# Kernel tuning notes

Measured on AMD Instinct MI355X. Metric: run time of the kernel, lower is better.

## Reference

```python
import jax, jax.numpy as jnp
import numpy as np

B, S, D, H = 4, 2048, 1024, 16
HS = D // H          # head size 64
DF = 4 * D           # ffn hidden 4096
EPS = 1e-5


def _layer_norm(x, g, b):
    mu = jnp.mean(x, axis=-1, keepdims=True)
    var = jnp.var(x, axis=-1, keepdims=True)
    return (x - mu) * jax.lax.rsqrt(var + EPS) * g + b


def setup_inputs() -> dict:
    key = jax.random.key(0)
    ks = jax.random.split(key, 12)
    s_d = 1.0 / np.sqrt(D)
    s_f = 1.0 / np.sqrt(DF)
    return {
        "x": jax.random.normal(ks[0], (B, S, D), jnp.float32),
        # per-head q/k/v projections, batched over heads: [H, D, HS]
        "wq": jax.random.uniform(ks[1], (H, D, HS), jnp.float32, -s_d, s_d),
        "wk": jax.random.uniform(ks[2], (H, D, HS), jnp.float32, -s_d, s_d),
        "wv": jax.random.uniform(ks[3], (H, D, HS), jnp.float32, -s_d, s_d),
        "proj_w": jax.random.uniform(ks[4], (D, D), jnp.float32, -s_d, s_d),
        "proj_b": jax.random.uniform(ks[5], (D,), jnp.float32, -s_d, s_d),
        "ff1_w": jax.random.uniform(ks[6], (D, DF), jnp.float32, -s_d, s_d),
        "ff1_b": jax.random.uniform(ks[7], (DF,), jnp.float32, -s_d, s_d),
        "ff2_w": jax.random.uniform(ks[8], (DF, D), jnp.float32, -s_f, s_f),
        "ff2_b": jax.random.uniform(ks[9], (D,), jnp.float32, -s_f, s_f),
        "ln1_g": jnp.ones((D,), jnp.float32),
        "ln1_b": jnp.zeros((D,), jnp.float32),
        "ln2_g": jnp.ones((D,), jnp.float32),
        "ln2_b": jnp.zeros((D,), jnp.float32),
    }


def reference(x, wq, wk, wv, proj_w, proj_b, ff1_w, ff1_b, ff2_w, ff2_b,
              ln1_g, ln1_b, ln2_g, ln2_b):
    # --- multi-head causal self-attention on ln1(x), all heads batched ---
    h = _layer_norm(x, ln1_g, ln1_b)                      # [B,S,D]
    q = jnp.einsum("bsd,hde->bhse", h, wq)                # [B,H,S,HS]
    k = jnp.einsum("bsd,hde->bhse", h, wk)
    v = jnp.einsum("bsd,hde->bhse", h, wv)
    scale = HS ** -0.5
    scores = jnp.einsum("bhse,bhte->bhst", q, k) * scale  # [B,H,S,S]
    causal = jnp.tril(jnp.ones((S, S), bool))
    scores = jnp.where(causal, scores, jnp.finfo(scores.dtype).min)
    att = jax.nn.softmax(scores, axis=-1)
    o = jnp.einsum("bhst,bhte->bhse", att, v)             # [B,H,S,HS]
    o = o.transpose(0, 2, 1, 3).reshape(B, S, D)          # concat heads
    sa = o @ proj_w + proj_b
    x = x + sa
    # --- FFN on ln2(x) ---
    h2 = _layer_norm(x, ln2_g, ln2_b)
    ff = jax.nn.relu(h2 @ ff1_w + ff1_b) @ ff2_w + ff2_b
    return x + ff
```

## Files before the change

kernel.cpp:

```cpp
#include <hip/hip_runtime.h>
#include <hip/hip_bf16.h>

#define BB 4
#define SS 2048
#define DD 1024
#define HH 16
#define HSZ 64
#define DFF 4096

typedef short short8 __attribute__((ext_vector_type(8)));
typedef float f32x4 __attribute__((ext_vector_type(4)));
typedef unsigned short us4 __attribute__((ext_vector_type(4)));

#define AS1 __attribute__((address_space(1)))
#define AS3 __attribute__((address_space(3)))

__device__ __forceinline__ unsigned short f2bf(float f) {
    return __bfloat16_as_ushort(__float2bfloat16(f));
}
__device__ __forceinline__ float bf2f(unsigned short u) {
    return __uint_as_float(((unsigned int)u) << 16);
}

__global__ __launch_bounds__(256) void pack_all_kernel(
    const float* __restrict__ wq, const float* __restrict__ wk,
    const float* __restrict__ wv, const float* __restrict__ proj_w,
    const float* __restrict__ ff1_w, const float* __restrict__ ff2_w,
    __hip_bfloat16* __restrict__ wqkvT, __hip_bfloat16* __restrict__ projT,
    __hip_bfloat16* __restrict__ ff1T, __hip_bfloat16* __restrict__ ff2T)
{
    __shared__ float tile[64][65];
    const int bid = blockIdx.x;
    const int tx = threadIdx.x & 63, ty = threadIdx.x >> 6;

    if (bid < 768) {
        const int kt = bid & 15, hh = (bid >> 4) & 15, sel = bid >> 8;
        const float* src = (sel == 0) ? wq : (sel == 1) ? wk : wv;
        src += (size_t)hh * (DD * HSZ) + (size_t)kt * 64 * HSZ;
        #pragma unroll
        for (int r = 0; r < 64; r += 4)
            tile[r + ty][tx] = src[(size_t)(r + ty) * HSZ + tx];
        __syncthreads();
        unsigned short* o = (unsigned short*)wqkvT + (size_t)(sel * DD + hh * 64) * DD + kt * 64;
        #pragma unroll
        for (int r = 0; r < 64; r += 4) {
            int e = r + ty;
            o[(size_t)e * DD + tx] = f2bf(tile[tx][e]);
        }
        return;
    }
    const float* in; unsigned short* o; int K, N, idx;
    if (bid < 1024)      { in = proj_w; o = (unsigned short*)projT; K = DD;  N = DD;  idx = bid - 768; }
    else if (bid < 2048) { in = ff1_w;  o = (unsigned short*)ff1T;  K = DD;  N = DFF; idx = bid - 1024; }
    else                 { in = ff2_w;  o = (unsigned short*)ff2T;  K = DFF; N = DD;  idx = bid - 2048; }
    const int nb = N >> 6;
    const int tn0 = (idx % nb) << 6, tk0 = (idx / nb) << 6;
    #pragma unroll
    for (int r = 0; r < 64; r += 4)
        tile[r + ty][tx] = in[(size_t)(tk0 + r + ty) * N + tn0 + tx];
    __syncthreads();
    #pragma unroll
    for (int r = 0; r < 64; r += 4) {
        int n = r + ty;
        o[(size_t)(tn0 + n) * K + tk0 + tx] = f2bf(tile[tx][n]);
    }
}

template<bool INBF16>
__global__ __launch_bounds__(256) void ln_kernel(
    const void* __restrict__ xin, const float* __restrict__ g,
    const float* __restrict__ b, __hip_bfloat16* __restrict__ out)
{
    int row = blockIdx.x;
    int t = threadIdx.x;
    float4 v;
    if (INBF16) {
        ushort4 u = ((const ushort4*)((const unsigned short*)xin + (size_t)row * DD))[t];
        v = make_float4(bf2f(u.x), bf2f(u.y), bf2f(u.z), bf2f(u.w));
    } else {
        v = ((const float4*)((const float*)xin + (size_t)row * DD))[t];
    }
    float s = v.x + v.y + v.z + v.w;
    float ss = v.x * v.x + v.y * v.y + v.z * v.z + v.w * v.w;
    #pragma unroll
    for (int off = 32; off; off >>= 1) {
        s += __shfl_xor(s, off, 64);
        ss += __shfl_xor(ss, off, 64);
    }
    __shared__ float red[8];
    int w = t >> 6, lane = t & 63;
    if (lane == 0) { red[w] = s; red[4 + w] = ss; }
    __syncthreads();
    s = red[0] + red[1] + red[2] + red[3];
    ss = red[4] + red[5] + red[6] + red[7];
    float mu = s * (1.f / DD);
    float var = ss * (1.f / DD) - mu * mu;
    float rs = rsqrtf(var + 1e-5f);
    float4 gv = ((const float4*)g)[t];
    float4 bv = ((const float4*)b)[t];
    ushort4 pk = make_ushort4(
        f2bf((v.x - mu) * rs * gv.x + bv.x),
        f2bf((v.y - mu) * rs * gv.y + bv.y),
        f2bf((v.z - mu) * rs * gv.z + bv.z),
        f2bf((v.w - mu) * rs * gv.w + bv.w));
    *(ushort4*)((unsigned short*)out + (size_t)row * DD + t * 4) = pk;
}

template<int BN, bool BIAS, bool RELU, bool RES, bool OUTF32, bool RESBF16>
__global__ __launch_bounds__(512) void gemm_kernel(
    const __hip_bfloat16* __restrict__ A, const __hip_bfloat16* __restrict__ BT,
    const float* __restrict__ bias, const void* __restrict__ res,
    void* __restrict__ Cout, int M, int N, int K, int nbx)
{
    constexpr int NB = BN / 128;
    constexpr int NREP = BN / 64;
    __shared__ uint4 Ah[2][2][1024];
    __shared__ uint4 Bh[2][NB][1024];

    const int tid = threadIdx.x;
    const int lane = tid & 63;
    const int w = tid >> 6;
    const int lr = lane & 15, g = lane >> 4;
    const int nwg = gridDim.x;
    const int cpx = nwg >> 3;
    const int wg = blockIdx.x;
    const int swz = (wg & 7) * cpx + (wg >> 3);
    const int bx = swz % nbx, by = swz / nbx;
    const int row0 = by * 256, col0 = bx * BN;
    const int wm = w >> 2, wn = w & 3;
    const int NT = K >> 6;

    f32x4 acc0[4][NREP] = {};
    f32x4 acc1[4][NREP] = {};
    short8 bfr[NREP][2];

    auto stageA = [&](int buf, int half, int t) {
        const int k0 = t * 64;
        #pragma unroll
        for (int j = 0; j < 2; ++j) {
            int s = j * 512 + tid;
            int r = s >> 3;
            int c = (s & 7) ^ (r & 7);
            const __hip_bfloat16* src = A + (size_t)(row0 + half * 128 + r) * K + k0 + c * 8;
            __builtin_amdgcn_global_load_lds((const AS1 void*)src,
                (AS3 void*)(&Ah[buf][half][j * 512 + (tid & ~63)]), 16, 0, 0);
        }
    };
    auto stageB = [&](int buf, int half, int t) {
        const int k0 = t * 64;
        #pragma unroll
        for (int j = 0; j < 2; ++j) {
            int s = j * 512 + tid;
            int r = s >> 3;
            int c = (s & 7) ^ (r & 7);
            const __hip_bfloat16* src = BT + (size_t)(col0 + half * 128 + r) * K + k0 + c * 8;
            __builtin_amdgcn_global_load_lds((const AS1 void*)src,
                (AS3 void*)(&Bh[buf][half][j * 512 + (tid & ~63)]), 16, 0, 0);
        }
    };
    auto loadB = [&](int buf) {
        const int hb = (NB == 2) ? (wn >> 1) : 0;
        const int cb = (NB == 2) ? ((wn & 1) * 64) : (wn * 32);
        #pragma unroll
        for (int n = 0; n < NREP; ++n) {
            int c = cb + n * 16 + lr;
            #pragma unroll
            for (int kk = 0; kk < 2; ++kk)
                bfr[n][kk] = *(const short8*)&Bh[buf][hb][c * 8 + ((kk * 4 + g) ^ (c & 7))];
        }
    };
    auto phase = [&](auto& acc, int buf, int mh) {
        short8 af[4][2];
        #pragma unroll
        for (int mi = 0; mi < 4; ++mi) {
            int r = wm * 64 + mi * 16 + lr;
            #pragma unroll
            for (int kk = 0; kk < 2; ++kk)
                af[mi][kk] = *(const short8*)&Ah[buf][mh][r * 8 + ((kk * 4 + g) ^ (r & 7))];
        }
        asm volatile("s_waitcnt lgkmcnt(0)" ::: "memory");
        __builtin_amdgcn_sched_barrier(0);
        __builtin_amdgcn_s_setprio(1);
        #pragma unroll
        for (int mi = 0; mi < 4; ++mi)
            #pragma unroll
            for (int n = 0; n < NREP; ++n)
                #pragma unroll
                for (int kk = 0; kk < 2; ++kk)
                    acc[mi][n] = __builtin_amdgcn_mfma_f32_16x16x32_bf16(
                        af[mi][kk], bfr[n][kk], acc[mi][n], 0, 0, 0);
        __builtin_amdgcn_s_setprio(0);
    };

    stageA(0, 0, 0);
    stageB(0, 0, 0);
    if constexpr (NB == 2) stageB(0, 1, 0);
    stageA(0, 1, 0);
    stageA(1, 0, 1);
    if constexpr (NB == 2) stageB(1, 0, 1);

    for (int t = 0; t < NT; ++t) {
        const int buf = t & 1;
        if (t < NT - 1) {
            if constexpr (NB == 2) asm volatile("s_waitcnt vmcnt(4)" ::: "memory");
            else                   asm volatile("s_waitcnt vmcnt(2)" ::: "memory");
        } else {
            asm volatile("s_waitcnt vmcnt(0)" ::: "memory");
        }
        __builtin_amdgcn_s_barrier();
        __builtin_amdgcn_sched_barrier(0);
        if (t + 1 < NT) {
            if constexpr (NB == 2) { stageB(buf ^ 1, 1, t + 1); stageA(buf ^ 1, 1, t + 1); }
            else                   { stageB(buf ^ 1, 0, t + 1); stageA(buf ^ 1, 1, t + 1); }
        }
        loadB(buf);
        phase(acc0, buf, 0);
        if (t < NT - 1) {
            if constexpr (NB == 2) asm volatile("s_waitcnt vmcnt(8)" ::: "memory");
            else                   asm volatile("s_waitcnt vmcnt(6)" ::: "memory");
        } else {
            asm volatile("s_waitcnt vmcnt(0)" ::: "memory");
        }
        __builtin_amdgcn_s_barrier();
        __builtin_amdgcn_sched_barrier(0);
        if (t + 2 < NT) {
            stageA(buf, 0, t + 2);
            if constexpr (NB == 2) stageB(buf, 0, t + 2);
        }
        phase(acc1, buf, 1);
    }

    auto store = [&](auto& acc, int mh) {
        #pragma unroll
        for (int mi = 0; mi < 4; ++mi) {
            #pragma unroll
            for (int j = 0; j < 4; ++j) {
                int rr = row0 + mh * 128 + wm * 64 + mi * 16 + g * 4 + j;
                #pragma unroll
                for (int n = 0; n < NREP; ++n) {
                    int cc = col0 + wn * (NREP * 16) + n * 16 + lr;
                    float vv = acc[mi][n][j];
                    if (BIAS) vv += bias[cc];
                    if (RELU) vv = fmaxf(vv, 0.f);
                    if (RES) {
                        if (RESBF16) vv += bf2f(((const unsigned short*)res)[(size_t)rr * N + cc]);
                        else         vv += ((const float*)res)[(size_t)rr * N + cc];
                    }
                    if (OUTF32) ((float*)Cout)[(size_t)rr * N + cc] = vv;
                    else ((__hip_bfloat16*)Cout)[(size_t)rr * N + cc] = __float2bfloat16(vv);
                }
            }
        }
    };
    store(acc0, 0);
    store(acc1, 1);
}

__device__ __forceinline__ void stage_K(
    const unsigned short* __restrict__ qkvu, size_t rowbase, int h, int kv0, int tl,
    unsigned short* __restrict__ Kb)
{
    int kv = tl >> 2, c = tl & 3;
    const unsigned short* src = qkvu + rowbase + (size_t)(kv0 + kv) * 3072 + DD + h * HSZ + c * 16;
    uint4 v0 = *(const uint4*)src;
    uint4 v1 = *(const uint4*)(src + 8);
    int sw = kv & 7;
    *(uint4*)&Kb[kv * 64 + ((2 * c) ^ sw) * 8] = v0;
    *(uint4*)&Kb[kv * 64 + ((2 * c + 1) ^ sw) * 8] = v1;
}

__device__ __forceinline__ void stage_V(
    const unsigned short* __restrict__ qkvu, size_t rowbase, int h, int kv0, int tl,
    unsigned short* __restrict__ Vb)
{
    int bkv = ((tl >> 6) << 2) | (tl & 3);
    int bd = (tl >> 2) & 15;
    const unsigned short* src = qkvu + rowbase + (size_t)(kv0 + bkv * 4) * 3072 + 2 * DD + h * HSZ + bd * 4;
    us4 r0 = *(const us4*)src;
    us4 r1 = *(const us4*)(src + 3072);
    us4 r2 = *(const us4*)(src + 2 * 3072);
    us4 r3 = *(const us4*)(src + 3 * 3072);
    #pragma unroll
    for (int cc = 0; cc < 4; ++cc) {
        int d = bd * 4 + cc;
        us4 wv = { r0[cc], r1[cc], r2[cc], r3[cc] };
        *(us4*)&Vb[d * 64 + (((bkv >> 1) ^ (d & 7)) * 8) + (bkv & 1) * 4] = wv;
    }
}

__device__ __forceinline__ void flash_tile(
    const unsigned short* __restrict__ Kb, const unsigned short* __restrict__ Vb,
    unsigned short* __restrict__ Pw, const short8* qfc, int qgc, int kv0, int q, int g,
    float& m_run, float& l_run, f32x4* oacc, bool masked)
{
    f32x4 st[4] = {};
    __builtin_amdgcn_s_setprio(1);
    #pragma unroll
    for (int tt = 0; tt < 4; ++tt) {
        #pragma unroll
        for (int kk = 0; kk < 2; ++kk) {
            short8 kf = *(const short8*)&Kb[(tt * 16 + q) * 64 + ((4 * kk + g) ^ (q & 7)) * 8];
            st[tt] = __builtin_amdgcn_mfma_f32_16x16x32_bf16(kf, qfc[kk], st[tt], 0, 0, 0);
        }
    }
    __builtin_amdgcn_s_setprio(0);

    const float SC = 0.1803368801111731f;
    float mt = -1e30f;
    if (masked) {
        #pragma unroll
        for (int tt = 0; tt < 4; ++tt)
            #pragma unroll
            for (int j = 0; j < 4; ++j) {
                float s = st[tt][j] * SC;
                int kvg = kv0 + tt * 16 + g * 4 + j;
                s = (kvg <= qgc) ? s : -1e30f;
                st[tt][j] = s;
                mt = fmaxf(mt, s);
            }
    } else {
        #pragma unroll
        for (int tt = 0; tt < 4; ++tt)
            #pragma unroll
            for (int j = 0; j < 4; ++j) {
                float s = st[tt][j] * SC;
                st[tt][j] = s;
                mt = fmaxf(mt, s);
            }
    }
    mt = fmaxf(mt, __shfl_xor(mt, 16, 64));
    mt = fmaxf(mt, __shfl_xor(mt, 32, 64));

    bool defer = __all(mt <= m_run + 11.0f);
    if (!defer) {
        float m_new = fmaxf(m_run, mt);
        float corr = exp2f(m_run - m_new);
        #pragma unroll
        for (int j = 0; j < 4; ++j) {
            float cj = __shfl(corr, g * 4 + j, 64);
            #pragma unroll
            for (int dn = 0; dn < 4; ++dn)
                oacc[dn][j] *= cj;
        }
        l_run *= corr;
        m_run = m_new;
    }

    float lsum = 0.f;
    #pragma unroll
    for (int tt = 0; tt < 4; ++tt)
        #pragma unroll
        for (int j = 0; j < 4; ++j) {
            float p = exp2f(st[tt][j] - m_run);
            st[tt][j] = p;
            lsum += p;
        }
    lsum += __shfl_xor(lsum, 16, 64);
    lsum += __shfl_xor(lsum, 32, 64);
    l_run += lsum;

    __builtin_amdgcn_s_setprio(1);
    #pragma unroll
    for (int kk = 0; kk < 2; ++kk) {
        #pragma unroll
        for (int rt = 0; rt < 2; ++rt) {
            int tt = kk * 2 + rt;
            unsigned int lo = ((unsigned int)f2bf(st[tt][1]) << 16) | (unsigned int)f2bf(st[tt][0]);
            unsigned int hi = ((unsigned int)f2bf(st[tt][3]) << 16) | (unsigned int)f2bf(st[tt][2]);
            uint2 pk = make_uint2(lo, hi);
            *(uint2*)&Pw[q * 32 + ((2 * rt + (g >> 1)) ^ ((q >> 1) & 3)) * 8 + (g & 1) * 4] = pk;
        }
        short8 pf = *(const short8*)&Pw[q * 32 + (g ^ ((q >> 1) & 3)) * 8];
        #pragma unroll
        for (int dn = 0; dn < 4; ++dn) {
            short8 vf = *(const short8*)&Vb[(dn * 16 + q) * 64 + ((4 * kk + g) ^ (q & 7)) * 8];
            oacc[dn] = __builtin_amdgcn_mfma_f32_16x16x32_bf16(pf, vf, oacc[dn], 0, 0, 0);
        }
    }
    __builtin_amdgcn_s_setprio(0);
}

__global__ __launch_bounds__(512, 4) void attn_kernel(
    const __hip_bfloat16* __restrict__ qkv, __hip_bfloat16* __restrict__ o)
{
    __shared__ unsigned short K_lds[2][2][64 * 64];
    __shared__ unsigned short Vt_lds[2][2][64 * 64];
    __shared__ unsigned short P_lds[8 * 512];

    const int t = threadIdx.x;
    const int lane = t & 63, w = t >> 6;
    const int grp = w >> 2, wq4 = w & 3, tl = t & 255;
    const int q = lane & 15, g = lane >> 4;
    const int wg = blockIdx.x;
    const int swzb = (wg & 7) * 128 + (wg >> 3);
    const int pq = swzb & 15;
    const int h = (swzb >> 4) & 15;
    const int b = swzb >> 8;
    const int qtA = pq, qtB = 31 - pq;
    const int qt1 = grp ? qtB : qtA;
    const unsigned short* qkvu = (const unsigned short*)qkv;
    const size_t rowbase = (size_t)(b * SS) * 3072;
    unsigned short* Pw = &P_lds[w * 512];
    unsigned short* op = (unsigned short*)o;

    int qt_cur = qt1;
    int qgc = qt_cur * 64 + wq4 * 16 + q;
    short8 qfc[2];
    #pragma unroll
    for (int kk = 0; kk < 2; ++kk)
        qfc[kk] = *(const short8*)(qkvu + rowbase + (size_t)qgc * 3072 + h * HSZ + kk * 32 + g * 8);

    f32x4 oacc[4] = {};
    float m_run = -1e30f, l_run = 0.f;

    const int P1 = (pq >> 1) + 1;
    for (int p = 0; p < P1; ++p) {
        const int t0 = 2 * p, t1 = 2 * p + 1;
        __syncthreads();
        if (grp == 0) {
            stage_K(qkvu, rowbase, h, t0 * 64, tl, K_lds[0][0]);
            stage_K(qkvu, rowbase, h, t1 * 64, tl, K_lds[0][1]);
        } else {
            stage_V(qkvu, rowbase, h, t0 * 64, tl, Vt_lds[0][0]);
            stage_V(qkvu, rowbase, h, t1 * 64, tl, Vt_lds[0][1]);
        }
        __syncthreads();
        flash_tile(K_lds[0][0], Vt_lds[0][0], Pw, qfc, qgc, t0 * 64, q, g, m_run, l_run, oacc,
                   t0 >= qt_cur);
        flash_tile(K_lds[0][1], Vt_lds[0][1], Pw, qfc, qgc, t1 * 64, q, g, m_run, l_run, oacc,
                   t1 >= qt_cur);
    }

    if (grp == 0) {
        #pragma unroll
        for (int j = 0; j < 4; ++j) {
            float lj = __shfl(l_run, g * 4 + j, 64);
            float inv = 1.f / lj;
            int orow = qtA * 64 + wq4 * 16 + g * 4 + j;
            #pragma unroll
            for (int dn = 0; dn < 4; ++dn)
                op[(size_t)(b * SS + orow) * DD + h * HSZ + dn * 16 + q] = f2bf(oacc[dn][j] * inv);
        }
        qt_cur = qtB;
        qgc = qtB * 64 + wq4 * 16 + q;
        #pragma unroll
        for (int kk = 0; kk < 2; ++kk)
            qfc[kk] = *(const short8*)(qkvu + rowbase + (size_t)qgc * 3072 + h * HSZ + kk * 32 + g * 8);
        m_run = -1e30f; l_run = 0.f;
        #pragma unroll
        for (int dn = 0; dn < 4; ++dn) oacc[dn] = f32x4{0.f, 0.f, 0.f, 0.f};
    }

    const int P2 = 8 - (pq >> 1);
    const int s1 = (pq | 1) + 1;
    for (int it2 = 0; it2 < P2; ++it2) {
        const int t0 = grp ? (s1 + 2 * it2) : (16 + 2 * it2);
        const int t1 = t0 + 1;
        const bool a0 = grp ? (t0 <= 15) : (t0 <= qtB);
        const bool a1 = grp ? (t1 <= 15) : (t1 <= qtB);
        __syncthreads();
        if (a0) {
            stage_K(qkvu, rowbase, h, t0 * 64, tl, K_lds[grp][0]);
            stage_V(qkvu, rowbase, h, t0 * 64, tl, Vt_lds[grp][0]);
        }
        if (a1) {
            stage_K(qkvu, rowbase, h, t1 * 64, tl, K_lds[grp][1]);
            stage_V(qkvu, rowbase, h, t1 * 64, tl, Vt_lds[grp][1]);
        }
        __syncthreads();
        if (a0) flash_tile(K_lds[grp][0], Vt_lds[grp][0], Pw, qfc, qgc, t0 * 64, q, g,
                           m_run, l_run, oacc, t0 >= qt_cur);
        if (a1) flash_tile(K_lds[grp][1], Vt_lds[grp][1], Pw, qfc, qgc, t1 * 64, q, g,
                           m_run, l_run, oacc, t1 >= qt_cur);
    }

    __syncthreads();
    float* obuf = (float*)K_lds;
    float* mlbuf = (float*)P_lds;
    if (grp == 0) {
        #pragma unroll
        for (int dn = 0; dn < 4; ++dn)
            #pragma unroll
            for (int j = 0; j < 4; ++j)
                obuf[wq4 * 1024 + lane * 16 + dn * 4 + j] = oacc[dn][j];
        if (g == 0) { mlbuf[wq4 * 32 + q] = m_run; mlbuf[wq4 * 32 + 16 + q] = l_run; }
    }
    __syncthreads();
    if (grp == 1) {
        float mA = mlbuf[wq4 * 32 + q];
        float lA = mlbuf[wq4 * 32 + 16 + q];
        float mM = fmaxf(m_run, mA);
        float sB = exp2f(m_run - mM);
        float sA = exp2f(mA - mM);
        float lM = l_run * sB + lA * sA;
        #pragma unroll
        for (int j = 0; j < 4; ++j) {
            float sBj = __shfl(sB, g * 4 + j, 64);
            float sAj = __shfl(sA, g * 4 + j, 64);
            float lMj = __shfl(lM, g * 4 + j, 64);
            float inv = 1.f / lMj;
            int orow = qtB * 64 + wq4 * 16 + g * 4 + j;
            #pragma unroll
            for (int dn = 0; dn < 4; ++dn) {
                float oA = obuf[wq4 * 1024 + lane * 16 + dn * 4 + j];
                float vv = (oacc[dn][j] * sBj + oA * sAj) * inv;
                op[(size_t)(b * SS + orow) * DD + h * HSZ + dn * 16 + q] = f2bf(vv);
            }
        }
    }
}

extern "C" void kernel_launch(void* const* d_in, const int* in_sizes, int n_in,
                              void* d_out, int out_size, void* d_ws, size_t ws_size,
                              hipStream_t stream)
{
    const float* x      = (const float*)d_in[0];
    const float* wq     = (const float*)d_in[1];
    const float* wk     = (const float*)d_in[2];
    const float* wv     = (const float*)d_in[3];
    const float* proj_w = (const float*)d_in[4];
    const float* proj_b = (const float*)d_in[5];
    const float* ff1_w  = (const float*)d_in[6];
    const float* ff1_b  = (const float*)d_in[7];
    const float* ff2_w  = (const float*)d_in[8];
    const float* ff2_b  = (const float*)d_in[9];
    const float* ln1_g  = (const float*)d_in[10];
    const float* ln1_b  = (const float*)d_in[11];
    const float* ln2_g  = (const float*)d_in[12];
    const float* ln2_b  = (const float*)d_in[13];
    float* out = (float*)d_out;

    char* ws = (char*)d_ws;
    const size_t MB = 1ull << 20;
    __hip_bfloat16* h     = (__hip_bfloat16*)(ws);
    __hip_bfloat16* qkv   = (__hip_bfloat16*)(ws + 16 * MB);
    __hip_bfloat16* obuf  = (__hip_bfloat16*)(ws + 64 * MB);
    __hip_bfloat16* x1b   = (__hip_bfloat16*)(ws + 80 * MB);
    __hip_bfloat16* wqkvT = (__hip_bfloat16*)(ws + 112 * MB);
    __hip_bfloat16* projT = (__hip_bfloat16*)(ws + 118 * MB);
    __hip_bfloat16* ff1T  = (__hip_bfloat16*)(ws + 120 * MB);
    __hip_bfloat16* ff2T  = (__hip_bfloat16*)(ws + 128 * MB);
    __hip_bfloat16* f1    = (__hip_bfloat16*)(ws + 16 * MB);

    const int ROWS = BB * SS;

    pack_all_kernel<<<3072, 256, 0, stream>>>(wq, wk, wv, proj_w, ff1_w, ff2_w,
                                              wqkvT, projT, ff1T, ff2T);

    ln_kernel<false><<<ROWS, 256, 0, stream>>>(x, ln1_g, ln1_b, h);
    gemm_kernel<128, false, false, false, false, false><<<(ROWS / 256) * (3 * DD / 128), 512, 0, stream>>>(
        h, wqkvT, nullptr, nullptr, qkv, ROWS, 3 * DD, DD, 3 * DD / 128);
    attn_kernel<<<BB * HH * 16, 512, 0, stream>>>(qkv, obuf);
    gemm_kernel<128, true, false, true, false, false><<<(ROWS / 256) * (DD / 128), 512, 0, stream>>>(
        obuf, projT, proj_b, x, x1b, ROWS, DD, DD, DD / 128);
    ln_kernel<true><<<ROWS, 256, 0, stream>>>(x1b, ln2_g, ln2_b, h);
    gemm_kernel<256, true, true, false, false, false><<<(ROWS / 256) * (DFF / 256), 512, 0, stream>>>(
        h, ff1T, ff1_b, nullptr, f1, ROWS, DFF, DD, DFF / 256);
    gemm_kernel<128, true, false, true, true, true><<<(ROWS / 256) * (DD / 128), 512, 0, stream>>>(
        f1, ff2T, ff2_b, x1b, out, ROWS, DD, DFF, DD / 128);
}
```

Before: 403.6 us.

## Prefetch next K/V tiles into registers during attention compute

Splits K/V staging into a global-to-register load and a register-to-LDS write, so the global loads for the next pair of KV tiles are issued before computing the current pair. The LDS write happens after a barrier, which hides global memory latency behind the MFMA and softmax work. The cost is extra registers holding prefetched tiles, which may lower occupancy. The loop now ends with a barrier, which replaces the one that preceded the epilogue.

New measurement: 428.0 us. +6.1%, slower.

```diff
diff --git a/kernel.cpp b/kernel.cpp
--- a/kernel.cpp
+++ b/kernel.cpp
@@ -256,34 +256,43 @@
     store(acc1, 1);
 }
 
-__device__ __forceinline__ void stage_K(
+__device__ __forceinline__ void load_K_regs(
     const unsigned short* __restrict__ qkvu, size_t rowbase, int h, int kv0, int tl,
-    unsigned short* __restrict__ Kb)
+    uint4& a, uint4& b)
 {
     int kv = tl >> 2, c = tl & 3;
     const unsigned short* src = qkvu + rowbase + (size_t)(kv0 + kv) * 3072 + DD + h * HSZ + c * 16;
-    uint4 v0 = *(const uint4*)src;
-    uint4 v1 = *(const uint4*)(src + 8);
-    int sw = kv & 7;
-    *(uint4*)&Kb[kv * 64 + ((2 * c) ^ sw) * 8] = v0;
-    *(uint4*)&Kb[kv * 64 + ((2 * c + 1) ^ sw) * 8] = v1;
-}
-
-__device__ __forceinline__ void stage_V(
+    a = *(const uint4*)src;
+    b = *(const uint4*)(src + 8);
+}
+__device__ __forceinline__ void write_K_lds(int tl, const uint4& a, const uint4& b,
+                                            unsigned short* __restrict__ Kb)
+{
+    int kv = tl >> 2, c = tl & 3, sw = kv & 7;
+    *(uint4*)&Kb[kv * 64 + ((2 * c) ^ sw) * 8] = a;
+    *(uint4*)&Kb[kv * 64 + ((2 * c + 1) ^ sw) * 8] = b;
+}
+__device__ __forceinline__ void load_V_regs(
     const unsigned short* __restrict__ qkvu, size_t rowbase, int h, int kv0, int tl,
-    unsigned short* __restrict__ Vb)
+    us4* r)
 {
     int bkv = ((tl >> 6) << 2) | (tl & 3);
     int bd = (tl >> 2) & 15;
     const unsigned short* src = qkvu + rowbase + (size_t)(kv0 + bkv * 4) * 3072 + 2 * DD + h * HSZ + bd * 4;
-    us4 r0 = *(const us4*)src;
-    us4 r1 = *(const us4*)(src + 3072);
-    us4 r2 = *(const us4*)(src + 2 * 3072);
-    us4 r3 = *(const us4*)(src + 3 * 3072);
+    r[0] = *(const us4*)src;
+    r[1] = *(const us4*)(src + 3072);
+    r[2] = *(const us4*)(src + 2 * 3072);
+    r[3] = *(const us4*)(src + 3 * 3072);
+}
+__device__ __forceinline__ void write_V_lds(int tl, const us4* r,
+                                            unsigned short* __restrict__ Vb)
+{
+    int bkv = ((tl >> 6) << 2) | (tl & 3);
+    int bd = (tl >> 2) & 15;
     #pragma unroll
     for (int cc = 0; cc < 4; ++cc) {
         int d = bd * 4 + cc;
-        us4 wv = { r0[cc], r1[cc], r2[cc], r3[cc] };
+        us4 wv = { r[0][cc], r[1][cc], r[2][cc], r[3][cc] };
         *(us4*)&Vb[d * 64 + (((bkv >> 1) ^ (d & 7)) * 8) + (bkv & 1) * 4] = wv;
     }
 }
@@ -413,22 +422,48 @@
     f32x4 oacc[4] = {};
     float m_run = -1e30f, l_run = 0.f;
 
+    uint4 kr0a, kr0b, kr1a, kr1b;
+    us4 vr0[4], vr1[4];
+
     const int P1 = (pq >> 1) + 1;
+    if (grp == 0) {
+        load_K_regs(qkvu, rowbase, h, 0, tl, kr0a, kr0b);
+        load_K_regs(qkvu, rowbase, h, 64, tl, kr1a, kr1b);
+        write_K_lds(tl, kr0a, kr0b, K_lds[0][0]);
+        write_K_lds(tl, kr1a, kr1b, K_lds[0][1]);
+    } else {
+        load_V_regs(qkvu, rowbase, h, 0, tl, vr0);
+        load_V_regs(qkvu, rowbase, h, 64, tl, vr1);
+        write_V_lds(tl, vr0, Vt_lds[0][0]);
+        write_V_lds(tl, vr1, Vt_lds[0][1]);
+    }
+    __syncthreads();
     for (int p = 0; p < P1; ++p) {
         const int t0 = 2 * p, t1 = 2 * p + 1;
-        __syncthreads();
-        if (grp == 0) {
-            stage_K(qkvu, rowbase, h, t0 * 64, tl, K_lds[0][0]);
-            stage_K(qkvu, rowbase, h, t1 * 64, tl, K_lds[0][1]);
-        } else {
-            stage_V(qkvu, rowbase, h, t0 * 64, tl, Vt_lds[0][0]);
-            stage_V(qkvu, rowbase, h, t1 * 64, tl, Vt_lds[0][1]);
-        }
-        __syncthreads();
+        if (p + 1 < P1) {
+            if (grp == 0) {
+                load_K_regs(qkvu, rowbase, h, (t0 + 2) * 64, tl, kr0a, kr0b);
+                load_K_regs(qkvu, rowbase, h, (t1 + 2) * 64, tl, kr1a, kr1b);
+            } else {
+                load_V_regs(qkvu, rowbase, h, (t0 + 2) * 64, tl, vr0);
+                load_V_regs(qkvu, rowbase, h, (t1 + 2) * 64, tl, vr1);
+            }
+        }
         flash_tile(K_lds[0][0], Vt_lds[0][0], Pw, qfc, qgc, t0 * 64, q, g, m_run, l_run, oacc,
                    t0 >= qt_cur);
         flash_tile(K_lds[0][1], Vt_lds[0][1], Pw, qfc, qgc, t1 * 64, q, g, m_run, l_run, oacc,
                    t1 >= qt_cur);
+        __syncthreads();
+        if (p + 1 < P1) {
+            if (grp == 0) {
+                write_K_lds(tl, kr0a, kr0b, K_lds[0][0]);
+                write_K_lds(tl, kr1a, kr1b, K_lds[0][1]);
+            } else {
+                write_V_lds(tl, vr0, Vt_lds[0][0]);
+                write_V_lds(tl, vr1, Vt_lds[0][1]);
+            }
+        }
+        __syncthreads();
     }
 
     if (grp == 0) {
@@ -453,28 +488,53 @@
 
     const int P2 = 8 - (pq >> 1);
     const int s1 = (pq | 1) + 1;
-    for (int it2 = 0; it2 < P2; ++it2) {
-        const int t0 = grp ? (s1 + 2 * it2) : (16 + 2 * it2);
-        const int t1 = t0 + 1;
-        const bool a0 = grp ? (t0 <= 15) : (t0 <= qtB);
-        const bool a1 = grp ? (t1 <= 15) : (t1 <= qtB);
+    unsigned short* Kb0 = K_lds[grp][0];
+    unsigned short* Kb1 = K_lds[grp][1];
+    unsigned short* Vb0 = Vt_lds[grp][0];
+    unsigned short* Vb1 = Vt_lds[grp][1];
+    auto tile0 = [&](int i) { return grp ? (s1 + 2 * i) : (16 + 2 * i); };
+    auto act = [&](int tt) { return grp ? (tt <= 15) : (tt <= qtB); };
+
+    {
+        int u0 = tile0(0), u1 = u0 + 1;
+        if (act(u0)) {
+            load_K_regs(qkvu, rowbase, h, u0 * 64, tl, kr0a, kr0b);
+            load_V_regs(qkvu, rowbase, h, u0 * 64, tl, vr0);
+            write_K_lds(tl, kr0a, kr0b, Kb0);
+            write_V_lds(tl, vr0, Vb0);
+        }
+        if (act(u1)) {
+            load_K_regs(qkvu, rowbase, h, u1 * 64, tl, kr1a, kr1b);
+            load_V_regs(qkvu, rowbase, h, u1 * 64, tl, vr1);
+            write_K_lds(tl, kr1a, kr1b, Kb1);
+            write_V_lds(tl, vr1, Vb1);
+        }
+    }
+    __syncthreads();
+    for (int i = 0; i < P2; ++i) {
+        const int u0 = tile0(i), u1 = u0 + 1;
+        const bool a0 = act(u0), a1 = act(u1);
+        const int n0 = tile0(i + 1), n1 = n0 + 1;
+        const bool pa0 = (i + 1 < P2) && act(n0);
+        const bool pa1 = (i + 1 < P2) && act(n1);
+        if (pa0) {
+            load_K_regs(qkvu, rowbase, h, n0 * 64, tl, kr0a, kr0b);
+            load_V_regs(qkvu, rowbase, h, n0 * 64, tl, vr0);
+        }
+        if (pa1) {
+            load_K_regs(qkvu, rowbase, h, n1 * 64, tl, kr1a, kr1b);
+            load_V_regs(qkvu, rowbase, h, n1 * 64, tl, vr1);
+        }
+        if (a0) flash_tile(Kb0, Vb0, Pw, qfc, qgc, u0 * 64, q, g, m_run, l_run, oacc,
+                           u0 >= qt_cur);
+        if (a1) flash_tile(Kb1, Vb1, Pw, qfc, qgc, u1 * 64, q, g, m_run, l_run, oacc,
+                           u1 >= qt_cur);
         __syncthreads();
-        if (a0) {
-            stage_K(qkvu, rowbase, h, t0 * 64, tl, K_lds[grp][0]);
-            stage_V(qkvu, rowbase, h, t0 * 64, tl, Vt_lds[grp][0]);
-        }
-        if (a1) {
-            stage_K(qkvu, rowbase, h, t1 * 64, tl, K_lds[grp][1]);
-            stage_V(qkvu, rowbase, h, t1 * 64, tl, Vt_lds[grp][1]);
-        }
+        if (pa0) { write_K_lds(tl, kr0a, kr0b, Kb0); write_V_lds(tl, vr0, Vb0); }
+        if (pa1) { write_K_lds(tl, kr1a, kr1b, Kb1); write_V_lds(tl, vr1, Vb1); }
         __syncthreads();
-        if (a0) flash_tile(K_lds[grp][0], Vt_lds[grp][0], Pw, qfc, qgc, t0 * 64, q, g,
-                           m_run, l_run, oacc, t0 >= qt_cur);
-        if (a1) flash_tile(K_lds[grp][1], Vt_lds[grp][1], Pw, qfc, qgc, t1 * 64, q, g,
-                           m_run, l_run, oacc, t1 >= qt_cur);
-    }
-
-    __syncthreads();
+    }
+
     float* obuf = (float*)K_lds;
     float* mlbuf = (float*)P_lds;
     if (grp == 0) {
```
